# Performance work log

Hardware: AMD Instinct MI355X
Metric: run time of the kernel (lower is better)

## Reference

```python
import jax, jax.numpy as jnp
import numpy as np

N = 50000      # nodes
E = 800000     # edges (avg degree 16)
LM = 1024      # lm_dim
H = 128        # hidden_channels
OUT = 64       # out_channels


def setup_inputs() -> dict:
    key = jax.random.key(0)
    ks = jax.random.split(key, 13)
    s = 0.02
    return {
        "x": jax.random.normal(ks[0], (N,), dtype=jnp.float32),
        "x_out": jax.random.normal(ks[1], (N, LM), dtype=jnp.float32),
        "c": jax.random.normal(ks[2], (N,), dtype=jnp.float32),
        "edge_index": jax.random.randint(ks[3], (2, E), 0, N, dtype=jnp.int64),
        "edge_weight": jax.random.uniform(ks[4], (E,), dtype=jnp.float32),
        # weights stored as [in, out]
        "Wa": jax.random.normal(ks[5], (1, LM), dtype=jnp.float32) * s,   # aa_linear (no bias)
        "Wc": jax.random.normal(ks[6], (1, LM), dtype=jnp.float32) * s,   # c_linear (no bias)
        "Wl": jax.random.normal(ks[7], (LM, LM), dtype=jnp.float32) * s,  # lm_linear
        "bl": jax.random.normal(ks[8], (LM,), dtype=jnp.float32) * s,
        "W1": jax.random.normal(ks[9], (LM, H), dtype=jnp.float32) * s,   # conv1
        "b1": jax.random.normal(ks[10], (H,), dtype=jnp.float32) * s,
        "W3": jax.random.normal(ks[11], (H, OUT), dtype=jnp.float32) * s,  # conv3
        "b3": jax.random.normal(ks[12], (OUT,), dtype=jnp.float32) * s,
    }


def gcn_conv(h, src, dst, ew, W, b, n):
    """PyG GCNConv with normalize=True, add_self_loops=True."""
    h = h @ W                                   # [n, out]
    loop = jnp.arange(n, dtype=src.dtype)
    src_f = jnp.concatenate([src, loop])
    dst_f = jnp.concatenate([dst, loop])
    ew_f = jnp.concatenate([ew, jnp.ones((n,), ew.dtype)])
    deg = jax.ops.segment_sum(ew_f, dst_f, num_segments=n)     # in-degree incl. self-loops
    dis = jnp.where(deg > 0, jax.lax.rsqrt(deg), 0.0)          # deg^{-1/2}
    norm = dis[src_f] * ew_f * dis[dst_f]                      # per-edge coefficient
    out = jax.ops.segment_sum(norm[:, None] * h[src_f], dst_f, num_segments=n)
    return out + b


def reference(x, x_out, c, edge_index, edge_weight, Wa, Wc, Wl, bl, W1, b1, W3, b3):
    # (c_linear(c[:,None]) + aa_linear(x[:,None]) + lm_linear(x_out)).relu()
    h = jax.nn.relu(c[:, None] * Wc[0] + x[:, None] * Wa[0] + x_out @ Wl + bl)  # [N, LM]
    src, dst = edge_index[0], edge_index[1]
    h = jax.nn.relu(gcn_conv(h, src, dst, edge_weight, W1, b1, N))              # [N, H]
    return gcn_conv(h, src, dst, edge_weight, W3, b3, N)                        # [N, OUT]
```

## Files before the change

kernel.cpp:

```cpp
#include <hip/hip_runtime.h>
#include <hip/hip_bf16.h>

typedef unsigned short u16;
typedef unsigned long long u64;
typedef __attribute__((ext_vector_type(8))) short bf16x8;
typedef __attribute__((ext_vector_type(4))) float f32x4;

constexpr int NN = 50000;
constexpr int NE = 800000;
constexpr int LM = 1024;
constexpr int HC = 128;
constexpr int OC = 64;

constexpr size_t OFF_ROWPTR = 0;
constexpr size_t OFF_CURSOR = 200192;
constexpr size_t OFF_PK     = 400384;
constexpr size_t OFF_INCL   = 800512;
constexpr size_t OFF_BSUM   = 1000704;
constexpr size_t OFF_DIS    = 1000960;
constexpr size_t OFF_META   = 1201152;
constexpr size_t OFF_WLT    = 7601408;
constexpr size_t OFF_W1T    = 9698560;
constexpr size_t OFF_H      = 9960704;
constexpr size_t OFF_Y1     = 112360704;
constexpr size_t OFF_Y3     = 125160704;
constexpr size_t OFF_ABF    = 131560704;
constexpr size_t NEED_FAST  = OFF_ABF + (size_t)NN * LM * 2;

__device__ __forceinline__ u16 f2bf(float f) {
    union { float f; unsigned int u; } a; a.f = f;
    unsigned int u = a.u + 0x7FFFu + ((a.u >> 16) & 1u);
    return (u16)(u >> 16);
}
__device__ __forceinline__ float bf2f(u16 v) {
    union { unsigned int u; float f; } a; a.u = ((unsigned int)v) << 16;
    return a.f;
}
__device__ __forceinline__ ushort2 pkbf(float a, float b) {
    union { __hip_bfloat162 h; ushort2 u; } cv;
    cv.h = __float22bfloat162_rn(make_float2(a, b));
    return cv.u;
}
__device__ __forceinline__ void async_copy16(u16* lds, const u16* g) {
    __builtin_amdgcn_global_load_lds(
        (const __attribute__((address_space(1))) void*)g,
        (__attribute__((address_space(3))) void*)lds, 16, 0, 0);
}

__global__ void k_setup(u64* __restrict__ pk,
                        const float* __restrict__ Wl, u16* __restrict__ WlT,
                        const float* __restrict__ W1, u16* __restrict__ W1T) {
    int b = blockIdx.x, t = threadIdx.x;
    if (b < 196) {
        int i = b * 256 + t;
        if (i < NN) pk[i] = 0ULL;
    } else if (b < 196 + 1024) {
        __shared__ float sm[32][33];
        int bb = b - 196;
        int n0 = (bb & 31) * 32, k0 = (bb >> 5) * 32;
        int ty = t >> 5, tx = t & 31;
        #pragma unroll
        for (int i = 0; i < 4; i++)
            sm[ty + i * 8][tx] = Wl[(size_t)(k0 + ty + i * 8) * LM + n0 + tx];
        __syncthreads();
        #pragma unroll
        for (int i = 0; i < 4; i++)
            WlT[(size_t)(n0 + ty + i * 8) * LM + k0 + tx] = f2bf(sm[tx][ty + i * 8]);
    } else {
        int idx = (b - 1220) * 256 + t;
        if (idx < HC * LM) {
            int o = idx >> 10, k = idx & 1023;
            W1T[idx] = f2bf(W1[(size_t)k * HC + o]);
        }
    }
}

__global__ void k_count(const int* __restrict__ ei, const float* __restrict__ ew,
                        u64* __restrict__ pk) {
    int e = blockIdx.x * 256 + threadIdx.x;
    if (e < NE) {
        int d = ei[NE + e];
        u64 add = (1ULL << 48) | (u64)(ew[e] * 4294967296.0);
        atomicAdd(&pk[d], add);
    }
}
__global__ void k_scan1(const u64* __restrict__ pk, int* __restrict__ incl,
                        int* __restrict__ bsum) {
    __shared__ int sm[1024];
    int t = threadIdx.x, idx = blockIdx.x * 1024 + t;
    int v = (idx < NN) ? (int)(pk[idx] >> 48) : 0;
    sm[t] = v; __syncthreads();
    for (int off = 1; off < 1024; off <<= 1) {
        int add = (t >= off) ? sm[t - off] : 0;
        __syncthreads();
        sm[t] += add;
        __syncthreads();
    }
    if (idx < NN) incl[idx] = sm[t];
    if (t == 1023) bsum[blockIdx.x] = sm[t];
}
__global__ void k_scan3(const int* __restrict__ incl, const u64* __restrict__ pk,
                        const int* __restrict__ bsum,
                        int* __restrict__ rowptr, int* __restrict__ cursor,
                        float* __restrict__ dis) {
    int seg = blockIdx.x >> 2;
    int lane = threadIdx.x & 63;
    int v = (lane < seg) ? bsum[lane] : 0;
    #pragma unroll
    for (int off = 32; off > 0; off >>= 1) v += __shfl_down(v, off, 64);
    int boffv = __shfl(v, 0, 64);
    int idx = blockIdx.x * 256 + threadIdx.x;
    if (idx < NN) {
        u64 p = pk[idx];
        int cnt = (int)(p >> 48);
        float deg = (float)((double)(p & 0xFFFFFFFFFFFFULL) * 2.3283064365386963e-10);
        int rp = incl[idx] - cnt + boffv;
        rowptr[idx] = rp;
        cursor[idx] = rp;
        dis[idx] = rsqrtf(1.0f + deg);
    } else if (idx == NN) {
        rowptr[NN] = NE;
    }
}
__global__ void k_fill(const int* __restrict__ ei, const float* __restrict__ ew,
                       const float* __restrict__ dis,
                       int* __restrict__ cursor, int2* __restrict__ meta) {
    int e = blockIdx.x * 256 + threadIdx.x;
    if (e < NE) {
        int s = ei[e];
        int d = ei[NE + e];
        int slot = atomicAdd(&cursor[d], 1);
        meta[slot] = make_int2(s, __float_as_int(ew[e] * dis[s]));
    }
}

__global__ __launch_bounds__(256) void k_cvtA(const float* __restrict__ A32,
                                              u16* __restrict__ Abf) {
    size_t idx = (size_t)blockIdx.x * 256 + threadIdx.x;
    const float* src = A32 + idx * 8;
    float4 v0 = *(const float4*)(src);
    float4 v1 = *(const float4*)(src + 4);
    union { ushort2 u2[4]; bf16x8 v; } pk;
    pk.u2[0] = pkbf(v0.x, v0.y);
    pk.u2[1] = pkbf(v0.z, v0.w);
    pk.u2[2] = pkbf(v1.x, v1.y);
    pk.u2[3] = pkbf(v1.z, v1.w);
    *(bf16x8*)(Abf + idx * 8) = pk.v;
}

__global__ __launch_bounds__(256, 2) void k_gemm1a(
    const u16* __restrict__ Abf, const u16* __restrict__ Bt, u16* __restrict__ Cout,
    const float* __restrict__ xv, const float* __restrict__ cv,
    const float* __restrict__ Wa, const float* __restrict__ Wc,
    const float* __restrict__ bl) {
    __shared__ u16 lA[128 * 64];
    __shared__ u16 lB[128 * 64];
    const int tid = threadIdx.x;
    const int lane = tid & 63, wv = tid >> 6;
    int x = blockIdx.x & 7, j = blockIdx.x >> 3;
    int bx = (j & ~7) | x;
    int by = j & 7;
    if (bx >= 391) return;
    const int m0 = bx * 128, n0 = by * 128;
    const int wm = (wv >> 1) * 64, wn = (wv & 1) * 64;
    const int fr = lane & 15, qd = lane >> 4;

    f32x4 acc[4][4] = {};

    for (int kt = 0; kt < 16; kt++) {
        const int k0 = kt << 6;
        __syncthreads();
        #pragma unroll
        for (int i = 0; i < 4; i++) {
            int r0 = i * 32 + wv * 8;
            int rl = r0 + (lane >> 3);
            int slot = lane & 7;
            int k8 = slot ^ (rl & 7);
            const u16* g = Bt + (size_t)(n0 + rl) * LM + k0 + k8 * 8;
            async_copy16(&lB[r0 * 64], g);
        }
        #pragma unroll
        for (int i = 0; i < 4; i++) {
            int r0 = i * 32 + wv * 8;
            int rl = r0 + (lane >> 3);
            int slot = lane & 7;
            int k8 = slot ^ (rl & 7);
            int row = m0 + rl; if (row >= NN) row = NN - 1;
            const u16* g = Abf + (size_t)row * LM + k0 + k8 * 8;
            async_copy16(&lA[r0 * 64], g);
        }
        __syncthreads();
        #pragma unroll
        for (int s = 0; s < 2; s++) {
            const int slot = (s * 4 + qd) ^ (fr & 7);
            bf16x8 af[4], bfm[4];
            #pragma unroll
            for (int mi = 0; mi < 4; mi++)
                af[mi] = *(const bf16x8*)&lA[(wm + mi * 16 + fr) * 64 + slot * 8];
            #pragma unroll
            for (int ni = 0; ni < 4; ni++)
                bfm[ni] = *(const bf16x8*)&lB[(wn + ni * 16 + fr) * 64 + slot * 8];
            #pragma unroll
            for (int mi = 0; mi < 4; mi++)
                #pragma unroll
                for (int ni = 0; ni < 4; ni++)
                    acc[mi][ni] = __builtin_amdgcn_mfma_f32_16x16x32_bf16(
                        af[mi], bfm[ni], acc[mi][ni], 0, 0, 0);
        }
    }

    int jj[4]; float waj[4], wcj[4], blj[4];
    #pragma unroll
    for (int ni = 0; ni < 4; ni++) {
        jj[ni] = n0 + wn + ni * 16 + fr;
        waj[ni] = Wa[jj[ni]]; wcj[ni] = Wc[jj[ni]]; blj[ni] = bl[jj[ni]];
    }
    #pragma unroll
    for (int mi = 0; mi < 4; mi++)
        #pragma unroll
        for (int r = 0; r < 4; r++) {
            int row = m0 + wm + mi * 16 + qd * 4 + r;
            if (row < NN) {
                float xb = xv[row], cb = cv[row];
                #pragma unroll
                for (int ni = 0; ni < 4; ni++) {
                    float v = acc[mi][ni][r] + xb * waj[ni] + cb * wcj[ni] + blj[ni];
                    Cout[(size_t)row * LM + jj[ni]] = f2bf(fmaxf(v, 0.f));
                }
            }
        }
}

__global__ __launch_bounds__(256, 2) void k_gemm1f(
    const float* __restrict__ A32, const u16* __restrict__ Bt, u16* __restrict__ Cout,
    const float* __restrict__ xv, const float* __restrict__ cv,
    const float* __restrict__ Wa, const float* __restrict__ Wc,
    const float* __restrict__ bl) {
    __shared__ u16 lA[128 * 64];
    __shared__ u16 lB[2][128 * 64];
    const int tid = threadIdx.x;
    const int lane = tid & 63, wv = tid >> 6;
    const int bx = ((blockIdx.x >> 5) << 3) | (blockIdx.x & 7);
    const int by = (blockIdx.x >> 3) & 3;
    if (bx >= 391) return;
    const int m0 = bx * 128, n0 = by * 256;
    const int wm = (wv >> 1) * 64, wn = (wv & 1) * 64;
    const int fr = lane & 15, qd = lane >> 4;

    f32x4 acc[2][4][4] = {};

    int srl[4], sslot[4]; const float* sbase[4];
    float4 pf[8];
    #pragma unroll
    for (int i = 0; i < 4; i++) {
        int cidx = i * 256 + tid;
        srl[i] = cidx >> 3; sslot[i] = cidx & 7;
        int k8 = sslot[i] ^ (srl[i] & 7);
        int row = m0 + srl[i]; if (row >= NN) row = NN - 1;
        sbase[i] = A32 + (size_t)row * LM + k8 * 8;
    }
    #pragma unroll
    for (int i = 0; i < 4; i++) {
        pf[2 * i]     = *(const float4*)(sbase[i]);
        pf[2 * i + 1] = *(const float4*)(sbase[i] + 4);
    }

    for (int kt = 0; kt < 16; kt++) {
        const int k0 = kt << 6;
        __syncthreads();
        #pragma unroll
        for (int h = 0; h < 2; h++)
            #pragma unroll
            for (int i = 0; i < 4; i++) {
                int r0 = i * 32 + wv * 8;
                int rl = r0 + (lane >> 3);
                int slot = lane & 7;
                int k8 = slot ^ (rl & 7);
                const u16* g = Bt + (size_t)(n0 + h * 128 + rl) * LM + k0 + k8 * 8;
                async_copy16(&lB[h][r0 * 64], g);
            }
        #pragma unroll
        for (int i = 0; i < 4; i++) {
            union { ushort2 u2[4]; bf16x8 v; } pk;
            pk.u2[0] = pkbf(pf[2 * i].x, pf[2 * i].y);
            pk.u2[1] = pkbf(pf[2 * i].z, pf[2 * i].w);
            pk.u2[2] = pkbf(pf[2 * i + 1].x, pf[2 * i + 1].y);
            pk.u2[3] = pkbf(pf[2 * i + 1].z, pf[2 * i + 1].w);
            *(bf16x8*)&lA[srl[i] * 64 + sslot[i] * 8] = pk.v;
        }
        __syncthreads();
        if (kt < 15) {
            #pragma unroll
            for (int i = 0; i < 4; i++) {
                pf[2 * i]     = *(const float4*)(sbase[i] + k0 + 64);
                pf[2 * i + 1] = *(const float4*)(sbase[i] + k0 + 68);
            }
        }
        #pragma unroll
        for (int s = 0; s < 2; s++) {
            const int slot = (s * 4 + qd) ^ (fr & 7);
            bf16x8 af[4];
            #pragma unroll
            for (int mi = 0; mi < 4; mi++)
                af[mi] = *(const bf16x8*)&lA[(wm + mi * 16 + fr) * 64 + slot * 8];
            #pragma unroll
            for (int h = 0; h < 2; h++) {
                bf16x8 bfm[4];
                #pragma unroll
                for (int ni = 0; ni < 4; ni++)
                    bfm[ni] = *(const bf16x8*)&lB[h][(wn + ni * 16 + fr) * 64 + slot * 8];
                #pragma unroll
                for (int mi = 0; mi < 4; mi++)
                    #pragma unroll
                    for (int ni = 0; ni < 4; ni++)
                        acc[h][mi][ni] = __builtin_amdgcn_mfma_f32_16x16x32_bf16(
                            af[mi], bfm[ni], acc[h][mi][ni], 0, 0, 0);
            }
        }
    }

    #pragma unroll
    for (int h = 0; h < 2; h++) {
        int jj[4]; float waj[4], wcj[4], blj[4];
        #pragma unroll
        for (int ni = 0; ni < 4; ni++) {
            jj[ni] = n0 + h * 128 + wn + ni * 16 + fr;
            waj[ni] = Wa[jj[ni]]; wcj[ni] = Wc[jj[ni]]; blj[ni] = bl[jj[ni]];
        }
        #pragma unroll
        for (int mi = 0; mi < 4; mi++)
            #pragma unroll
            for (int r = 0; r < 4; r++) {
                int row = m0 + wm + mi * 16 + qd * 4 + r;
                if (row < NN) {
                    float xb = xv[row], cb = cv[row];
                    #pragma unroll
                    for (int ni = 0; ni < 4; ni++) {
                        float v = acc[h][mi][ni][r] + xb * waj[ni] + cb * wcj[ni] + blj[ni];
                        Cout[(size_t)row * LM + jj[ni]] = f2bf(fmaxf(v, 0.f));
                    }
                }
            }
    }
}

__global__ __launch_bounds__(256) void k_gemm2(
    const u16* __restrict__ Abf, const u16* __restrict__ Bt, u16* __restrict__ Cout) {
    __shared__ u16 lA[64 * 64];
    __shared__ u16 lB[128 * 64];
    const int tid = threadIdx.x;
    const int lane = tid & 63, wv = tid >> 6;
    const int m0 = blockIdx.x * 64;
    const int wm = (wv >> 1) * 32, wn = (wv & 1) * 64;
    const int fr = lane & 15, qd = lane >> 4;
    f32x4 acc[2][4] = {};

    for (int kt = 0; kt < 16; kt++) {
        const int k0 = kt << 6;
        __syncthreads();
        #pragma unroll
        for (int i = 0; i < 4; i++) {
            int r0 = i * 32 + wv * 8;
            int rl = r0 + (lane >> 3);
            int slot = lane & 7;
            int k8 = slot ^ (rl & 7);
            const u16* g = Bt + (size_t)rl * LM + k0 + k8 * 8;
            async_copy16(&lB[r0 * 64], g);
        }
        #pragma unroll
        for (int i = 0; i < 2; i++) {
            int r0 = i * 32 + wv * 8;
            int rl = r0 + (lane >> 3);
            int slot = lane & 7;
            int k8 = slot ^ (rl & 7);
            int row = m0 + rl; if (row >= NN) row = NN - 1;
            const u16* g = Abf + (size_t)row * LM + k0 + k8 * 8;
            async_copy16(&lA[r0 * 64], g);
        }
        __syncthreads();
        #pragma unroll
        for (int s = 0; s < 2; s++) {
            const int slot = (s * 4 + qd) ^ (fr & 7);
            bf16x8 af[2], bfm[4];
            #pragma unroll
            for (int mi = 0; mi < 2; mi++)
                af[mi] = *(const bf16x8*)&lA[(wm + mi * 16 + fr) * 64 + slot * 8];
            #pragma unroll
            for (int ni = 0; ni < 4; ni++)
                bfm[ni] = *(const bf16x8*)&lB[(wn + ni * 16 + fr) * 64 + slot * 8];
            #pragma unroll
            for (int mi = 0; mi < 2; mi++)
                #pragma unroll
                for (int ni = 0; ni < 4; ni++)
                    acc[mi][ni] = __builtin_amdgcn_mfma_f32_16x16x32_bf16(
                        af[mi], bfm[ni], acc[mi][ni], 0, 0, 0);
        }
    }
    #pragma unroll
    for (int mi = 0; mi < 2; mi++)
        #pragma unroll
        for (int r = 0; r < 4; r++) {
            int row = m0 + wm + mi * 16 + qd * 4 + r;
            if (row < NN) {
                #pragma unroll
                for (int ni = 0; ni < 4; ni++)
                    Cout[(size_t)row * HC + wn + ni * 16 + fr] = f2bf(acc[mi][ni][r]);
            }
        }
}

__global__ __launch_bounds__(512) void k_agg1g3(
    const u16* __restrict__ y1, const int* __restrict__ rowptr,
    const int2* __restrict__ meta, const float* __restrict__ dis,
    const float* __restrict__ b1, const float* __restrict__ W3,
    u16* __restrict__ y3) {
    __shared__ float hrow[8][HC];
    int wv = threadIdx.x >> 6, lane = threadIdx.x & 63;
    int node = blockIdx.x * 8 + wv;
    if (node >= NN) return;
    float di = dis[node];
    int p0 = rowptr[node], p1 = rowptr[node + 1];
    ushort2 sv = *(const ushort2*)(y1 + (size_t)node * HC + lane * 2);
    float a0 = di * bf2f(sv.x), a1 = di * bf2f(sv.y);
    #pragma unroll 8
    for (int p = p0; p < p1; ++p) {
        int2 m = meta[p];
        float nm = __int_as_float(m.y);
        ushort2 v = *(const ushort2*)(y1 + (size_t)m.x * HC + lane * 2);
        a0 += nm * bf2f(v.x);
        a1 += nm * bf2f(v.y);
    }
    a0 = fmaxf(di * a0 + b1[lane * 2], 0.f);
    a1 = fmaxf(di * a1 + b1[lane * 2 + 1], 0.f);
    hrow[wv][lane * 2] = a0;
    hrow[wv][lane * 2 + 1] = a1;
    float acc = 0.f;
    #pragma unroll 8
    for (int k = 0; k < HC; ++k)
        acc += hrow[wv][k] * W3[(size_t)k * OC + lane];
    y3[(size_t)node * OC + lane] = f2bf(acc);
}

__global__ __launch_bounds__(256) void k_agg3(
    const u16* __restrict__ y3, const int* __restrict__ rowptr,
    const int2* __restrict__ meta, const float* __restrict__ dis,
    const float* __restrict__ b3, float* __restrict__ outp) {
    int node = blockIdx.x * 4 + (threadIdx.x >> 6);
    int lane = threadIdx.x & 63;
    if (node >= NN) return;
    float di = dis[node];
    int p0 = rowptr[node], p1 = rowptr[node + 1];
    float a = di * bf2f(y3[(size_t)node * OC + lane]);
    #pragma unroll 8
    for (int p = p0; p < p1; ++p) {
        int2 m = meta[p];
        a += __int_as_float(m.y) * bf2f(y3[(size_t)m.x * OC + lane]);
    }
    outp[(size_t)node * OC + lane] = di * a + b3[lane];
}

extern "C" void kernel_launch(void* const* d_in, const int* in_sizes, int n_in,
                              void* d_out, int out_size, void* d_ws, size_t ws_size,
                              hipStream_t stream) {
    const float* x    = (const float*)d_in[0];
    const float* xout = (const float*)d_in[1];
    const float* c    = (const float*)d_in[2];
    const int*   ei   = (const int*)d_in[3];
    const float* ew   = (const float*)d_in[4];
    const float* Wa   = (const float*)d_in[5];
    const float* Wc   = (const float*)d_in[6];
    const float* Wl   = (const float*)d_in[7];
    const float* bl   = (const float*)d_in[8];
    const float* W1   = (const float*)d_in[9];
    const float* b1   = (const float*)d_in[10];
    const float* W3   = (const float*)d_in[11];
    const float* b3   = (const float*)d_in[12];
    float* outp = (float*)d_out;

    char* ws = (char*)d_ws;
    int*   rowptr = (int*)(ws + OFF_ROWPTR);
    int*   cursor = (int*)(ws + OFF_CURSOR);
    u64*   pk     = (u64*)(ws + OFF_PK);
    int*   incl   = (int*)(ws + OFF_INCL);
    int*   bsum   = (int*)(ws + OFF_BSUM);
    float* dis    = (float*)(ws + OFF_DIS);
    int2*  meta   = (int2*)(ws + OFF_META);
    u16*   WlT    = (u16*)(ws + OFF_WLT);
    u16*   W1T    = (u16*)(ws + OFF_W1T);
    u16*   hbuf   = (u16*)(ws + OFF_H);
    u16*   y1     = (u16*)(ws + OFF_Y1);
    u16*   y3     = (u16*)(ws + OFF_Y3);
    u16*   Abf    = (u16*)(ws + OFF_ABF);

    k_setup<<<1732, 256, 0, stream>>>(pk, Wl, WlT, W1, W1T);
    k_count<<<3125, 256, 0, stream>>>(ei, ew, pk);
    k_scan1<<<49, 1024, 0, stream>>>(pk, incl, bsum);
    k_scan3<<<196, 256, 0, stream>>>(incl, pk, bsum, rowptr, cursor, dis);
    k_fill <<<3125, 256, 0, stream>>>(ei, ew, dis, cursor, meta);

    if (ws_size >= NEED_FAST) {
        k_cvtA  <<<25000, 256, 0, stream>>>(xout, Abf);
        k_gemm1a<<<392 * 8, 256, 0, stream>>>(Abf, WlT, hbuf, x, c, Wa, Wc, bl);
    } else {
        k_gemm1f<<<49 * 32, 256, 0, stream>>>(xout, WlT, hbuf, x, c, Wa, Wc, bl);
    }
    k_gemm2<<<782, 256, 0, stream>>>(hbuf, W1T, y1);
    k_agg1g3<<<6250, 512, 0, stream>>>(y1, rowptr, meta, dis, b1, W3, y3);
    k_agg3<<<12500, 256, 0, stream>>>(y3, rowptr, meta, dis, b3, outp);
}
```

Baseline: 666.0 us.

## Replace lm_linear GEMM with 4-stage pipelined 128x256-tile 512-thread kernel

The lm_linear GEMM kernel is rewritten to use 512-thread blocks computing 128x256 output tiles with a K-step of 32. It runs a 4-buffer LDS ring where loads for step t+3 are issued before the MFMAs of step t, gated by vmcnt waits and raw barriers. MFMA sections run with raised wave priority, and the LDS swizzle changes to suit the narrower K-slab. The aim is to hide global-to-LDS latency and increase B reuse per block. In exchange, the larger LDS footprint likely limits occupancy to one block per CU.

```diff
diff --git a/kernel.cpp b/kernel.cpp
--- a/kernel.cpp
+++ b/kernel.cpp
@@ -148,66 +148,86 @@
     *(bf16x8*)(Abf + idx * 8) = pk.v;
 }
 
-__global__ __launch_bounds__(256, 2) void k_gemm1a(
+constexpr int BKD = 32;
+constexpr int NTK = LM / BKD;
+constexpr int BUFW = (128 + 256) * BKD;
+
+__global__ __launch_bounds__(512, 2) void k_gemm1b(
     const u16* __restrict__ Abf, const u16* __restrict__ Bt, u16* __restrict__ Cout,
     const float* __restrict__ xv, const float* __restrict__ cv,
     const float* __restrict__ Wa, const float* __restrict__ Wc,
     const float* __restrict__ bl) {
-    __shared__ u16 lA[128 * 64];
-    __shared__ u16 lB[128 * 64];
+    __shared__ u16 lds[4][BUFW];
     const int tid = threadIdx.x;
     const int lane = tid & 63, wv = tid >> 6;
-    int x = blockIdx.x & 7, j = blockIdx.x >> 3;
-    int bx = (j & ~7) | x;
-    int by = j & 7;
-    if (bx >= 391) return;
-    const int m0 = bx * 128, n0 = by * 128;
-    const int wm = (wv >> 1) * 64, wn = (wv & 1) * 64;
     const int fr = lane & 15, qd = lane >> 4;
+    int wgid = (blockIdx.x & 7) * 196 + (blockIdx.x >> 3);
+    const int bx = wgid >> 2, by = wgid & 3;
+    const int m0 = bx * 128, n0 = by * 256;
+    const int wm = (wv >> 2) * 64, wn = (wv & 3) * 64;
+    const int sk = (qd ^ ((fr >> 1) & 3)) * 8;
+
+    const int srow = lane >> 2;
+    const int sslot = lane & 3;
 
     f32x4 acc[4][4] = {};
 
-    for (int kt = 0; kt < 16; kt++) {
-        const int k0 = kt << 6;
-        __syncthreads();
-        #pragma unroll
-        for (int i = 0; i < 4; i++) {
-            int r0 = i * 32 + wv * 8;
-            int rl = r0 + (lane >> 3);
-            int slot = lane & 7;
-            int k8 = slot ^ (rl & 7);
-            const u16* g = Bt + (size_t)(n0 + rl) * LM + k0 + k8 * 8;
-            async_copy16(&lB[r0 * 64], g);
-        }
-        #pragma unroll
-        for (int i = 0; i < 4; i++) {
-            int r0 = i * 32 + wv * 8;
-            int rl = r0 + (lane >> 3);
-            int slot = lane & 7;
-            int k8 = slot ^ (rl & 7);
-            int row = m0 + rl; if (row >= NN) row = NN - 1;
-            const u16* g = Abf + (size_t)row * LM + k0 + k8 * 8;
-            async_copy16(&lA[r0 * 64], g);
-        }
-        __syncthreads();
-        #pragma unroll
-        for (int s = 0; s < 2; s++) {
-            const int slot = (s * 4 + qd) ^ (fr & 7);
-            bf16x8 af[4], bfm[4];
-            #pragma unroll
-            for (int mi = 0; mi < 4; mi++)
-                af[mi] = *(const bf16x8*)&lA[(wm + mi * 16 + fr) * 64 + slot * 8];
+    auto stageA = [&](int ks, int st) {
+        int rl = wv * 16 + srow;
+        int row = m0 + rl; if (row >= NN) row = NN - 1;
+        int k8 = sslot ^ ((rl >> 1) & 3);
+        const u16* g = Abf + (size_t)row * LM + ks * BKD + k8 * 8;
+        async_copy16(&lds[st][(wv * 16) * BKD], g);
+    };
+    auto stageB = [&](int ks, int st) {
+        #pragma unroll
+        for (int i = 0; i < 2; i++) {
+            int r0 = wv * 32 + i * 16;
+            int rl = r0 + srow;
+            int k8 = sslot ^ ((rl >> 1) & 3);
+            const u16* g = Bt + (size_t)(n0 + rl) * LM + ks * BKD + k8 * 8;
+            async_copy16(&lds[st][128 * BKD + r0 * BKD], g);
+        }
+    };
+
+    stageA(0, 0); stageB(0, 0);
+    stageA(1, 1); stageB(1, 1);
+    stageA(2, 2); stageB(2, 2);
+    asm volatile("s_waitcnt vmcnt(6)" ::: "memory");
+    __builtin_amdgcn_s_barrier();
+    asm volatile("" ::: "memory");
+
+    for (int t = 0; t < NTK; t++) {
+        const u16* bA = &lds[t & 3][0];
+        const u16* bB = &lds[t & 3][128 * BKD];
+        bf16x8 af[4], bf[4];
+        #pragma unroll
+        for (int mi = 0; mi < 4; mi++)
+            af[mi] = *(const bf16x8*)&bA[(wm + mi * 16 + fr) * BKD + sk];
+        #pragma unroll
+        for (int ni = 0; ni < 4; ni++)
+            bf[ni] = *(const bf16x8*)&bB[(wn + ni * 16 + fr) * BKD + sk];
+        int ks = (t + 3 < NTK) ? t + 3 : NTK - 1;
+        int st = (t + 3) & 3;
+        stageA(ks, st);
+        stageB(ks, st);
+        asm volatile("s_waitcnt vmcnt(6)" ::: "memory");
+        __builtin_amdgcn_s_barrier();
+        asm volatile("" ::: "memory");
+        __builtin_amdgcn_s_setprio(1);
+        #pragma unroll
+        for (int mi = 0; mi < 4; mi++)
             #pragma unroll
             for (int ni = 0; ni < 4; ni++)
-                bfm[ni] = *(const bf16x8*)&lB[(wn + ni * 16 + fr) * 64 + slot * 8];
-            #pragma unroll
-            for (int mi = 0; mi < 4; mi++)
-                #pragma unroll
-                for (int ni = 0; ni < 4; ni++)
-                    acc[mi][ni] = __builtin_amdgcn_mfma_f32_16x16x32_bf16(
-                        af[mi], bfm[ni], acc[mi][ni], 0, 0, 0);
-        }
-    }
+                acc[mi][ni] = __builtin_amdgcn_mfma_f32_16x16x32_bf16(
+                    af[mi], bf[ni], acc[mi][ni], 0, 0, 0);
+        __builtin_amdgcn_s_setprio(0);
+        asm volatile("" ::: "memory");
+        __builtin_amdgcn_s_barrier();
+        asm volatile("" ::: "memory");
+    }
+
+    asm volatile("s_waitcnt vmcnt(0)" ::: "memory");
 
     int jj[4]; float waj[4], wcj[4], blj[4];
     #pragma unroll
@@ -500,7 +520,7 @@
 
     if (ws_size >= NEED_FAST) {
         k_cvtA  <<<25000, 256, 0, stream>>>(xout, Abf);
-        k_gemm1a<<<392 * 8, 256, 0, stream>>>(Abf, WlT, hbuf, x, c, Wa, Wc, bl);
+        k_gemm1b<<<392 * 4, 512, 0, stream>>>(Abf, WlT, hbuf, x, c, Wa, Wc, bl);
     } else {
         k_gemm1f<<<49 * 32, 256, 0, stream>>>(xout, WlT, hbuf, x, c, Wa, Wc, bl);
     }
```

Result: slower. 735.3 us (+10.4%).
